# Performance work log

Measured on AMD Instinct MI355X. Metric: run time of the kernel, lower is better.

The kernel has to match this reference:

```python
import jax, jax.numpy as jnp
import numpy as np

D_MODEL = 1024
EXPAND = 2
D_INNER = EXPAND * D_MODEL   # 2048
D_STATE = 16
D_CONV = 4
DT_RANK = 64                  # ceil(d_model / 16)
BATCH = 2
SEQLEN = 1024
DT_MIN, DT_MAX = 0.001, 0.1


def setup_inputs() -> dict:
    key = jax.random.key(0)
    ks = jax.random.split(key, 10)
    s = 0.02
    # dt bias init per Mamba: inv-softplus of dt sampled log-uniform in [dt_min, dt_max]
    u = jax.random.uniform(ks[0], (D_INNER,), jnp.float32)
    dt = jnp.exp(u * (np.log(DT_MAX) - np.log(DT_MIN)) + np.log(DT_MIN))
    dt = jnp.clip(dt, 1e-4, None)
    inv_dt = dt + jnp.log(-jnp.expm1(-dt))
    dt_std = DT_RANK ** -0.5
    A_log = jnp.log(jnp.tile(jnp.arange(1, D_STATE + 1, dtype=jnp.float32), (D_INNER, 1)))
    return {
        "hidden_states": jax.random.normal(ks[1], (BATCH, SEQLEN, D_MODEL), jnp.float32),
        "in_proj_w": jax.random.normal(ks[2], (2 * D_INNER, D_MODEL), jnp.float32) * s,
        "conv1d_w": jax.random.normal(ks[3], (D_INNER, D_CONV), jnp.float32) * s,
        "conv1d_b": jnp.zeros((D_INNER,), jnp.float32),
        "x_proj_w": jax.random.normal(ks[4], (DT_RANK + 2 * D_STATE, D_INNER), jnp.float32) * s,
        "dt_proj_w": jax.random.uniform(ks[5], (D_INNER, DT_RANK), jnp.float32, -dt_std, dt_std),
        "dt_proj_b": inv_dt,
        "A_log": A_log,
        "D_skip": jnp.ones((D_INNER,), jnp.float32),
        "out_proj_w": jax.random.normal(ks[6], (D_MODEL, D_INNER), jnp.float32) * s,
    }


def _mamba_forward(hidden_states, in_proj_w, conv1d_w, conv1d_b, x_proj_w,
                   dt_proj_w, dt_proj_b, A_log, D_skip, out_proj_w):
    B_, L, _ = hidden_states.shape
    # in_proj: (b, l, d_model) -> (b, l, 2*d_inner); split into x and gate z
    xz = jnp.einsum('bld,ed->ble', hidden_states, in_proj_w)
    x, z = xz[..., :D_INNER], xz[..., D_INNER:]
    # causal depthwise conv1d over time (pad left K-1, truncate to L) + SiLU
    xp = jnp.pad(x, ((0, 0), (D_CONV - 1, 0), (0, 0)))
    xc = conv1d_b
    acc = jnp.zeros_like(x)
    for k in range(D_CONV):  # tiny fixed kernel loop
        acc = acc + conv1d_w[:, k] * xp[:, k:k + L, :]
    xc = jax.nn.silu(acc + conv1d_b)
    # input-dependent dt / B / C
    x_dbl = jnp.einsum('bld,rd->blr', xc, x_proj_w)
    dt_lr = x_dbl[..., :DT_RANK]
    Bm = x_dbl[..., DT_RANK:DT_RANK + D_STATE]        # (b, l, n)
    Cm = x_dbl[..., DT_RANK + D_STATE:]               # (b, l, n)
    delta = jax.nn.softplus(jnp.einsum('blr,dr->bld', dt_lr, dt_proj_w) + dt_proj_b)
    A = -jnp.exp(A_log)                               # (d, n)

    def step(state, inputs):
        delta_t, B_t, C_t, u_t = inputs               # (b,d) (b,n) (b,n) (b,d)
        dA = jnp.exp(delta_t[..., None] * A)          # (b, d, n)
        state = state * dA + (delta_t * u_t)[..., None] * B_t[:, None, :]
        y_t = jnp.einsum('bdn,bn->bd', state, C_t)
        return state, y_t

    init = jnp.zeros((B_, D_INNER, D_STATE), delta.dtype)
    scan_in = (jnp.swapaxes(delta, 0, 1), jnp.swapaxes(Bm, 0, 1),
               jnp.swapaxes(Cm, 0, 1), jnp.swapaxes(xc, 0, 1))
    _, ys = jax.lax.scan(step, init, scan_in)         # ys: (l, b, d)
    y = jnp.swapaxes(ys, 0, 1)
    y = y + xc * D_skip                               # skip connection
    y = y * jax.nn.silu(z)                            # gate
    return jnp.einsum('bld,md->blm', y, out_proj_w)   # out_proj (no bias)


def reference(hidden_states, in_proj_w, conv1d_w, conv1d_b, x_proj_w,
              dt_proj_w, dt_proj_b, A_log, D_skip, out_proj_w):
    return _mamba_forward(hidden_states, in_proj_w, conv1d_w, conv1d_b, x_proj_w,
                          dt_proj_w, dt_proj_b, A_log, D_skip, out_proj_w)
```

## Files before the change

### kernel.cpp

```cpp
#include <hip/hip_runtime.h>
#include <hip/hip_bf16.h>
#include <math.h>
#include <stdint.h>

#define D_MODEL 1024
#define D_INNER 2048
#define D_STATE 16
#define D_CONV  4
#define DT_RANK 64
#define BATCH   2
#define SEQLEN  1024
#define M_TOK   (BATCH * SEQLEN)
#define XDBL_W  (DT_RANK + 2 * D_STATE)
#define CHUNKS  64
#define CLEN    (SEQLEN / CHUNKS)
#define KSPLIT  32
#define OSPLIT  4

typedef unsigned short us16;
typedef __bf16 bf16x8 __attribute__((ext_vector_type(8)));
typedef float floatx4 __attribute__((ext_vector_type(4)));

__device__ __forceinline__ float silu_f(float v) {
    return v / (1.0f + __expf(-v));
}
__device__ __forceinline__ float softplus_f(float v) {
    return v > 20.0f ? v : log1pf(__expf(v));
}
__device__ __forceinline__ us16 f2bf(float f) {
    unsigned u = __float_as_uint(f);
    u += 0x7FFF + ((u >> 16) & 1);
    return (us16)(u >> 16);
}
__device__ __forceinline__ float bf2f(us16 h) {
    return __uint_as_float(((unsigned)h) << 16);
}

__device__ __forceinline__ void gload_lds16(const us16* g, us16* l) {
    auto* l3 = reinterpret_cast<__attribute__((address_space(3))) us16*>(
        reinterpret_cast<uintptr_t>(l));
    auto* g1 = reinterpret_cast<const __attribute__((address_space(1))) us16*>(
        reinterpret_cast<uintptr_t>(g));
    __builtin_amdgcn_global_load_lds(g1, l3, 16, 0, 0);
}

__global__ __launch_bounds__(256)
void split_all(const float* __restrict__ hs, const float* __restrict__ iw,
               const float* __restrict__ ow,
               us16* __restrict__ hsh, us16* __restrict__ hsl,
               us16* __restrict__ iwh, us16* __restrict__ iwl,
               us16* __restrict__ owh, us16* __restrict__ owl)
{
    const int b = blockIdx.x;
    const float* src;
    us16 *hi, *lo;
    int rel;
    if (b < 2048)      { src = hs; hi = hsh; lo = hsl; rel = b; }
    else if (b < 6144) { src = iw; hi = iwh; lo = iwl; rel = b - 2048; }
    else               { src = ow; hi = owh; lo = owl; rel = b - 6144; }
    const int i = (rel * 256 + threadIdx.x) * 4;
    const float4 v = *(const float4*)(src + i);
    us16 h0 = f2bf(v.x), h1 = f2bf(v.y), h2 = f2bf(v.z), h3 = f2bf(v.w);
    ushort4 hv = {h0, h1, h2, h3};
    ushort4 lv = {f2bf(v.x - bf2f(h0)), f2bf(v.y - bf2f(h1)),
                  f2bf(v.z - bf2f(h2)), f2bf(v.w - bf2f(h3))};
    *(ushort4*)(hi + i) = hv;
    *(ushort4*)(lo + i) = lv;
}

template<int BN, int MODE>
__global__ __launch_bounds__(256)
void gemm_mfma3(const us16* __restrict__ Ah, const us16* __restrict__ Al,
                const us16* __restrict__ Wh, const us16* __restrict__ Wl,
                int lda, int kLen, float* __restrict__ C0,
                float* __restrict__ C1, int ldc)
{
    constexpr int BM = 128;
    constexpr int NT = BN / 32;
    __shared__ us16 sAh[BM * 32];
    __shared__ us16 sAl[BM * 32];
    __shared__ us16 sWh[BN * 32];
    __shared__ us16 sWl[BN * 32];

    const int tid  = threadIdx.x;
    const int wave = tid >> 6;
    const int lane = tid & 63;
    const int wm   = wave & 1;
    const int wn   = wave >> 1;
    const int m0   = blockIdx.y * BM;
    const int n0   = blockIdx.x * BN;
    const int kBeg = blockIdx.z * kLen;
    const int quad = lane >> 4;
    const int l15  = lane & 15;
    const int sr   = lane >> 2;
    const int spos = lane & 3;

    floatx4 acc[4][NT] = {};

    for (int k0 = 0; k0 < kLen; k0 += 32) {
        __syncthreads();
        {
            int s = wave;
            int row = s * 16 + sr;
            int c = spos ^ ((row >> 1) & 3);
            size_t go = (size_t)(m0 + row) * lda + kBeg + k0 + c * 8;
            gload_lds16(Ah + go, sAh + s * 512);
            gload_lds16(Al + go, sAl + s * 512);
            s = wave + 4;
            row = s * 16 + sr;
            c = spos ^ ((row >> 1) & 3);
            go = (size_t)(m0 + row) * lda + kBeg + k0 + c * 8;
            gload_lds16(Ah + go, sAh + s * 512);
            gload_lds16(Al + go, sAl + s * 512);
        }
        {
            int s = wave;
            int row = s * 16 + sr;
            int c = spos ^ ((row >> 1) & 3);
            size_t go = (size_t)(n0 + row) * lda + kBeg + k0 + c * 8;
            gload_lds16(Wh + go, sWh + s * 512);
            gload_lds16(Wl + go, sWl + s * 512);
            if (BN == 128) {
                s = wave + 4;
                row = s * 16 + sr;
                c = spos ^ ((row >> 1) & 3);
                go = (size_t)(n0 + row) * lda + kBeg + k0 + c * 8;
                gload_lds16(Wh + go, sWh + s * 512);
                gload_lds16(Wl + go, sWl + s * 512);
            }
        }
        __syncthreads();

        bf16x8 ah[4], al[4], bh[NT], bl[NT];
#pragma unroll
        for (int i = 0; i < 4; i++) {
            const int r = wm * 64 + i * 16 + l15;
            const int off = r * 32 + ((quad ^ ((r >> 1) & 3)) * 8);
            ah[i] = *(const bf16x8*)(sAh + off);
            al[i] = *(const bf16x8*)(sAl + off);
        }
#pragma unroll
        for (int j = 0; j < NT; j++) {
            const int r = wn * (BN / 2) + j * 16 + l15;
            const int off = r * 32 + ((quad ^ ((r >> 1) & 3)) * 8);
            bh[j] = *(const bf16x8*)(sWh + off);
            bl[j] = *(const bf16x8*)(sWl + off);
        }
#pragma unroll
        for (int i = 0; i < 4; i++)
#pragma unroll
            for (int j = 0; j < NT; j++) {
                acc[i][j] = __builtin_amdgcn_mfma_f32_16x16x32_bf16(
                    ah[i], bh[j], acc[i][j], 0, 0, 0);
                acc[i][j] = __builtin_amdgcn_mfma_f32_16x16x32_bf16(
                    al[i], bh[j], acc[i][j], 0, 0, 0);
                acc[i][j] = __builtin_amdgcn_mfma_f32_16x16x32_bf16(
                    ah[i], bl[j], acc[i][j], 0, 0, 0);
            }
    }

#pragma unroll
    for (int i = 0; i < 4; i++) {
        const int rowb = m0 + wm * 64 + i * 16 + quad * 4;
#pragma unroll
        for (int j = 0; j < NT; j++) {
            const int col = n0 + wn * (BN / 2) + j * 16 + l15;
#pragma unroll
            for (int r = 0; r < 4; r++) {
                const float v = acc[i][j][r];
                const size_t rr = (size_t)(rowb + r);
                if (MODE == 1) {
                    if (n0 < D_INNER) C0[rr * D_INNER + col] = v;
                    else              C1[rr * D_INNER + (col - D_INNER)] = v;
                } else {
                    C0[((size_t)blockIdx.z * M_TOK + rr) * ldc + col] = v;
                }
            }
        }
    }
}

__global__ __launch_bounds__(256)
void add4_kernel(const float* __restrict__ part, float* __restrict__ out)
{
    const int i = (blockIdx.x * 256 + threadIdx.x) * 4;
    const size_t stride = (size_t)M_TOK * D_MODEL;
    float4 a = *(const float4*)(part + i);
#pragma unroll
    for (int k = 1; k < OSPLIT; k++) {
        const float4 b = *(const float4*)(part + k * stride + i);
        a.x += b.x; a.y += b.y; a.z += b.z; a.w += b.w;
    }
    *(float4*)(out + i) = a;
}

__global__ __launch_bounds__(256)
void gemm_dt(const float* __restrict__ A, int lda,
             const float* __restrict__ W, int ldw,
             float* __restrict__ C0, int ldc,
             const float* __restrict__ bias, int K)
{
    __shared__ float As[16][68];
    __shared__ float Ws[16][68];

    const int tid  = threadIdx.x;
    const int tx   = tid & 15;
    const int ty   = tid >> 4;
    const int n0   = blockIdx.x * 64;
    const int m0   = blockIdx.y * 64;
    const int lrow = tid >> 2;
    const int lkq  = tid & 3;

    float acc[4][4] = {};

    for (int k0 = 0; k0 < K; k0 += 16) {
        const float4 av = *(const float4*)(A + (size_t)(m0 + lrow) * lda + k0 + lkq * 4);
        const float4 wv = *(const float4*)(W + (size_t)(n0 + lrow) * ldw + k0 + lkq * 4);

        __syncthreads();
        As[lkq * 4 + 0][lrow] = av.x;
        As[lkq * 4 + 1][lrow] = av.y;
        As[lkq * 4 + 2][lrow] = av.z;
        As[lkq * 4 + 3][lrow] = av.w;
        Ws[lkq * 4 + 0][lrow] = wv.x;
        Ws[lkq * 4 + 1][lrow] = wv.y;
        Ws[lkq * 4 + 2][lrow] = wv.z;
        Ws[lkq * 4 + 3][lrow] = wv.w;
        __syncthreads();

#pragma unroll
        for (int k = 0; k < 16; k++) {
            const float4 a = *(const float4*)&As[k][ty * 4];
            const float4 w = *(const float4*)&Ws[k][tx * 4];
            const float avv[4] = {a.x, a.y, a.z, a.w};
            const float wvv[4] = {w.x, w.y, w.z, w.w};
#pragma unroll
            for (int i = 0; i < 4; i++)
#pragma unroll
                for (int j = 0; j < 4; j++)
                    acc[i][j] += avv[i] * wvv[j];
        }
    }

    const int mbase = m0 + ty * 4;
    const int nbase = n0 + tx * 4;
#pragma unroll
    for (int i = 0; i < 4; i++)
#pragma unroll
        for (int j = 0; j < 4; j++) {
            const int n = nbase + j;
            C0[(size_t)(mbase + i) * ldc + n] = softplus_f(acc[i][j] + bias[n]);
        }
}

__global__ __launch_bounds__(256)
void gemm_xproj(const float* __restrict__ xg, const float* __restrict__ conv_w,
                const float* __restrict__ conv_b,
                const float* __restrict__ W, float* __restrict__ part)
{
    __shared__ float As[16][68];
    __shared__ float Ws[16][100];

    const int tid  = threadIdx.x;
    const int tx   = tid & 15;
    const int ty   = tid >> 4;
    const int m0   = blockIdx.x * 64;
    const int kz   = blockIdx.y;
    const int lrow = tid >> 2;
    const int lkq  = tid & 3;

    const float4* cw = (const float4*)conv_w;
    const float4* cb = (const float4*)conv_b;

    float acc[4][6] = {};
    const int kbeg = kz * (D_INNER / KSPLIT);
    const int kend = kbeg + (D_INNER / KSPLIT);

    const int m = m0 + lrow;
    const int t = m & (SEQLEN - 1);

    for (int k0 = kbeg; k0 < kend; k0 += 16) {
        const int dcol = k0 + lkq * 4;
        const float4 w0 = cw[dcol], w1 = cw[dcol + 1], w2 = cw[dcol + 2], w3 = cw[dcol + 3];
        float4 a = cb[dcol >> 2];
        const float* xr = xg + (size_t)m * D_INNER + dcol;
        {
            float4 xk;
            if (t >= 3) { xk = *(const float4*)(xr - 3 * D_INNER);
                a.x += w0.x * xk.x; a.y += w1.x * xk.y; a.z += w2.x * xk.z; a.w += w3.x * xk.w; }
            if (t >= 2) { xk = *(const float4*)(xr - 2 * D_INNER);
                a.x += w0.y * xk.x; a.y += w1.y * xk.y; a.z += w2.y * xk.z; a.w += w3.y * xk.w; }
            if (t >= 1) { xk = *(const float4*)(xr - 1 * D_INNER);
                a.x += w0.z * xk.x; a.y += w1.z * xk.y; a.z += w2.z * xk.z; a.w += w3.z * xk.w; }
            xk = *(const float4*)(xr);
            a.x += w0.w * xk.x; a.y += w1.w * xk.y; a.z += w2.w * xk.z; a.w += w3.w * xk.w;
        }
        const float4 av = make_float4(silu_f(a.x), silu_f(a.y), silu_f(a.z), silu_f(a.w));

        const float4 wv = *(const float4*)(W + (size_t)lrow * D_INNER + k0 + lkq * 4);
        float4 wv2 = make_float4(0.f, 0.f, 0.f, 0.f);
        if (tid < 128)
            wv2 = *(const float4*)(W + (size_t)(64 + lrow) * D_INNER + k0 + lkq * 4);

        __syncthreads();
        As[lkq * 4 + 0][lrow] = av.x;
        As[lkq * 4 + 1][lrow] = av.y;
        As[lkq * 4 + 2][lrow] = av.z;
        As[lkq * 4 + 3][lrow] = av.w;
        Ws[lkq * 4 + 0][lrow] = wv.x;
        Ws[lkq * 4 + 1][lrow] = wv.y;
        Ws[lkq * 4 + 2][lrow] = wv.z;
        Ws[lkq * 4 + 3][lrow] = wv.w;
        if (tid < 128) {
            Ws[lkq * 4 + 0][64 + lrow] = wv2.x;
            Ws[lkq * 4 + 1][64 + lrow] = wv2.y;
            Ws[lkq * 4 + 2][64 + lrow] = wv2.z;
            Ws[lkq * 4 + 3][64 + lrow] = wv2.w;
        }
        __syncthreads();

#pragma unroll
        for (int k = 0; k < 16; k++) {
            const float4 a4 = *(const float4*)&As[k][ty * 4];
            const float avv[4] = {a4.x, a4.y, a4.z, a4.w};
            float wvv[6];
#pragma unroll
            for (int j = 0; j < 6; j++) wvv[j] = Ws[k][tx * 6 + j];
#pragma unroll
            for (int i = 0; i < 4; i++)
#pragma unroll
                for (int j = 0; j < 6; j++)
                    acc[i][j] += avv[i] * wvv[j];
        }
    }

    const int mbase = m0 + ty * 4;
    const int nbase = tx * 6;
#pragma unroll
    for (int i = 0; i < 4; i++)
#pragma unroll
        for (int j = 0; j < 6; j++)
            part[((size_t)kz * M_TOK + mbase + i) * XDBL_W + nbase + j] = acc[i][j];
}

__global__ __launch_bounds__(256)
void xproj_reduce(const float* __restrict__ part, float* __restrict__ xdbl)
{
    const int i = blockIdx.x * 256 + threadIdx.x;
    float s = 0.f;
#pragma unroll 8
    for (int k = 0; k < KSPLIT; k++)
        s += part[(size_t)k * M_TOK * XDBL_W + i];
    xdbl[i] = s;
}

__global__ __launch_bounds__(256)
void scan_part(const float* __restrict__ delta, const float* __restrict__ xdbl,
               const float* __restrict__ xg, const float* __restrict__ conv_w,
               const float* __restrict__ conv_b, const float* __restrict__ A_log,
               float* __restrict__ P, float* __restrict__ S)
{
    const int g = blockIdx.x * 256 + threadIdx.x;
    const int d = g & (D_INNER - 1);
    const int c = (g >> 11) & (CHUNKS - 1);
    const int b = g >> 17;

    float An[D_STATE];
#pragma unroll
    for (int n = 0; n < D_STATE; n++)
        An[n] = -__expf(A_log[d * D_STATE + n]);

    const float4 wd = ((const float4*)conv_w)[d];
    const float cb = conv_b[d];

    float p[D_STATE], s[D_STATE];
#pragma unroll
    for (int n = 0; n < D_STATE; n++) { p[n] = 1.f; s[n] = 0.f; }

    const size_t row0 = (size_t)b * SEQLEN + c * CLEN;
    const float* xp = xg + row0 * D_INNER + d;
    float xm3 = 0.f, xm2 = 0.f, xm1 = 0.f;
    if (c > 0) {
        xm3 = xp[-3 * D_INNER];
        xm2 = xp[-2 * D_INNER];
        xm1 = xp[-1 * D_INNER];
    }

#pragma unroll 4
    for (int t = 0; t < CLEN; t++) {
        const size_t row = row0 + t;
        const float xm0 = xp[(size_t)t * D_INNER];
        const float u   = silu_f(cb + wd.x * xm3 + wd.y * xm2 + wd.z * xm1 + wd.w * xm0);
        xm3 = xm2; xm2 = xm1; xm1 = xm0;
        const float dlt  = delta[row * D_INNER + d];
        const float dltu = dlt * u;
        const float4* Bp = (const float4*)(xdbl + row * XDBL_W + DT_RANK);
        const float4 B0 = Bp[0], B1 = Bp[1], B2 = Bp[2], B3 = Bp[3];
        const float Bv[D_STATE] = {B0.x, B0.y, B0.z, B0.w, B1.x, B1.y, B1.z, B1.w,
                                   B2.x, B2.y, B2.z, B2.w, B3.x, B3.y, B3.z, B3.w};
#pragma unroll
        for (int n = 0; n < D_STATE; n++) {
            const float a = __expf(dlt * An[n]);
            s[n] = s[n] * a + dltu * Bv[n];
            p[n] *= a;
        }
    }

    const size_t base = ((size_t)(b * CHUNKS + c) * D_STATE) * D_INNER + d;
#pragma unroll
    for (int n = 0; n < D_STATE; n++) {
        P[base + (size_t)n * D_INNER] = p[n];
        S[base + (size_t)n * D_INNER] = s[n];
    }
}

__global__ __launch_bounds__(256)
void scan_prefix(float* PH, const float* __restrict__ S)
{
    const int g = blockIdx.x * 256 + threadIdx.x;
    const int d = g & (D_INNER - 1);
    const int n = (g >> 11) & (D_STATE - 1);
    const int b = g >> 15;

    float h = 0.f;
    for (int c = 0; c < CHUNKS; c++) {
        const size_t idx = ((size_t)(b * CHUNKS + c) * D_STATE + n) * D_INNER + d;
        const float p = PH[idx];
        const float s = S[idx];
        PH[idx] = h;
        h = s + p * h;
    }
}

__global__ __launch_bounds__(256)
void scan_apply(const float* __restrict__ delta, const float* __restrict__ xdbl,
                const float* __restrict__ xg, const float* __restrict__ conv_w,
                const float* __restrict__ conv_b, const float* __restrict__ A_log,
                const float* __restrict__ D_skip,
                const float* __restrict__ H,
                const float* __restrict__ z,
                us16* __restrict__ yh, us16* __restrict__ yl)
{
    const int g = blockIdx.x * 256 + threadIdx.x;
    const int d = g & (D_INNER - 1);
    const int c = (g >> 11) & (CHUNKS - 1);
    const int b = g >> 17;

    float An[D_STATE];
#pragma unroll
    for (int n = 0; n < D_STATE; n++)
        An[n] = -__expf(A_log[d * D_STATE + n]);

    const float4 wd = ((const float4*)conv_w)[d];
    const float cb = conv_b[d];

    float st[D_STATE];
    const size_t hbase = ((size_t)(b * CHUNKS + c) * D_STATE) * D_INNER + d;
#pragma unroll
    for (int n = 0; n < D_STATE; n++)
        st[n] = H[hbase + (size_t)n * D_INNER];

    const float Dv = D_skip[d];
    const size_t row0 = (size_t)b * SEQLEN + c * CLEN;
    const float* xp = xg + row0 * D_INNER + d;
    float xm3 = 0.f, xm2 = 0.f, xm1 = 0.f;
    if (c > 0) {
        xm3 = xp[-3 * D_INNER];
        xm2 = xp[-2 * D_INNER];
        xm1 = xp[-1 * D_INNER];
    }

#pragma unroll 4
    for (int t = 0; t < CLEN; t++) {
        const size_t row = row0 + t;
        const float xm0 = xp[(size_t)t * D_INNER];
        const float u   = silu_f(cb + wd.x * xm3 + wd.y * xm2 + wd.z * xm1 + wd.w * xm0);
        xm3 = xm2; xm2 = xm1; xm1 = xm0;
        const float dlt  = delta[row * D_INNER + d];
        const float dltu = dlt * u;
        const float4* Bp = (const float4*)(xdbl + row * XDBL_W + DT_RANK);
        const float4 B0 = Bp[0], B1 = Bp[1], B2 = Bp[2], B3 = Bp[3];
        const float4* Cp = (const float4*)(xdbl + row * XDBL_W + DT_RANK + D_STATE);
        const float4 C0 = Cp[0], C1 = Cp[1], C2 = Cp[2], C3 = Cp[3];
        const float Bv[D_STATE] = {B0.x, B0.y, B0.z, B0.w, B1.x, B1.y, B1.z, B1.w,
                                   B2.x, B2.y, B2.z, B2.w, B3.x, B3.y, B3.z, B3.w};
        const float Cv[D_STATE] = {C0.x, C0.y, C0.z, C0.w, C1.x, C1.y, C1.z, C1.w,
                                   C2.x, C2.y, C2.z, C2.w, C3.x, C3.y, C3.z, C3.w};
        float y = 0.f;
#pragma unroll
        for (int n = 0; n < D_STATE; n++) {
            const float a = __expf(dlt * An[n]);
            st[n] = st[n] * a + dltu * Bv[n];
            y += st[n] * Cv[n];
        }
        const float yv = (y + u * Dv) * silu_f(z[row * D_INNER + d]);
        const us16 h = f2bf(yv);
        yh[row * D_INNER + d] = h;
        yl[row * D_INNER + d] = f2bf(yv - bf2f(h));
    }
}

extern "C" void kernel_launch(void* const* d_in, const int* in_sizes, int n_in,
                              void* d_out, int out_size, void* d_ws, size_t ws_size,
                              hipStream_t stream)
{
    const float* hs         = (const float*)d_in[0];
    const float* in_proj_w  = (const float*)d_in[1];
    const float* conv_w     = (const float*)d_in[2];
    const float* conv_b     = (const float*)d_in[3];
    const float* x_proj_w   = (const float*)d_in[4];
    const float* dt_proj_w  = (const float*)d_in[5];
    const float* dt_proj_b  = (const float*)d_in[6];
    const float* A_log      = (const float*)d_in[7];
    const float* D_skip     = (const float*)d_in[8];
    const float* out_proj_w = (const float*)d_in[9];
    float* out = (float*)d_out;

    char* base = (char*)d_ws;
    const size_t MB = 1u << 20;
    float* xbuf  = (float*)(base);
    float* zbuf  = (float*)(base + 16 * MB);
    float* opart = (float*)(base);
    float* dbuf  = (float*)(base + 32 * MB);
    float* xdbl  = (float*)(base + 48 * MB);
    us16*  iwh   = (us16*)(base + 49 * MB);
    us16*  iwl   = (us16*)(base + 57 * MB);
    float* part  = (float*)(base + 49 * MB);
    float* Pbuf  = (float*)(base + 49 * MB);
    us16*  hsh   = (us16*)(base + 65 * MB);
    us16*  hsl   = (us16*)(base + 69 * MB);
    float* Sbuf  = (float*)(base + 65 * MB);
    us16*  ybh   = (us16*)(base + 65 * MB);
    us16*  ybl   = (us16*)(base + 73 * MB);
    us16*  owh   = (us16*)(base + 81 * MB);
    us16*  owl   = (us16*)(base + 85 * MB);

    const dim3 blk(256);

    split_all<<<8192, blk, 0, stream>>>(hs, in_proj_w, out_proj_w,
                                        hsh, hsl, iwh, iwl, owh, owl);

    gemm_mfma3<64, 1><<<dim3((2 * D_INNER) / 64, M_TOK / 128), blk, 0, stream>>>(
        hsh, hsl, iwh, iwl, D_MODEL, D_MODEL, xbuf, zbuf, D_INNER);

    gemm_xproj<<<dim3(M_TOK / 64, KSPLIT), blk, 0, stream>>>(
        xbuf, conv_w, conv_b, x_proj_w, part);
    xproj_reduce<<<(M_TOK * XDBL_W) / 256, blk, 0, stream>>>(part, xdbl);

    gemm_dt<<<dim3(D_INNER / 64, M_TOK / 64), blk, 0, stream>>>(
        xdbl, XDBL_W, dt_proj_w, DT_RANK, dbuf, D_INNER, dt_proj_b, DT_RANK);

    scan_part<<<(BATCH * CHUNKS * D_INNER) / 256, blk, 0, stream>>>(
        dbuf, xdbl, xbuf, conv_w, conv_b, A_log, Pbuf, Sbuf);
    scan_prefix<<<(BATCH * D_STATE * D_INNER) / 256, blk, 0, stream>>>(
        Pbuf, Sbuf);
    scan_apply<<<(BATCH * CHUNKS * D_INNER) / 256, blk, 0, stream>>>(
        dbuf, xdbl, xbuf, conv_w, conv_b, A_log, D_skip, Pbuf, zbuf, ybh, ybl);

    gemm_mfma3<128, 2><<<dim3(D_MODEL / 128, M_TOK / 128, OSPLIT), blk, 0, stream>>>(
        ybh, ybl, owh, owl, D_INNER, D_INNER / OSPLIT, opart, nullptr, D_MODEL);
    add4_kernel<<<(M_TOK * D_MODEL) / 1024, blk, 0, stream>>>(opart, out);
}
```

Baseline: 323.6 us.

## Replace split-K partial buffers and reduce kernels with atomic accumulation

The out_proj and x_proj split-K GEMMs now accumulate straight into the output and xdbl with float atomicAdd, after a new kernel zeroes both buffers. This removes the add4 and xproj_reduce kernels and their partial-buffer traffic. The in_proj GEMM also moves from a 64-wide to a 128-wide N tile, giving fewer blocks with more reuse. In exchange, the 32-way atomic contention on the small xdbl buffer may be costly, and the summation order is no longer deterministic.

```diff
diff --git a/kernel.cpp b/kernel.cpp
--- a/kernel.cpp
+++ b/kernel.cpp
@@ -42,6 +42,19 @@
     auto* g1 = reinterpret_cast<const __attribute__((address_space(1))) us16*>(
         reinterpret_cast<uintptr_t>(g));
     __builtin_amdgcn_global_load_lds(g1, l3, 16, 0, 0);
+}
+
+__global__ __launch_bounds__(256)
+void zero_kernel(float* __restrict__ out, float* __restrict__ xdbl)
+{
+    const int b = blockIdx.x;
+    if (b < 2048) {
+        const int i = (b * 256 + threadIdx.x) * 4;
+        *(float4*)(out + i) = make_float4(0.f, 0.f, 0.f, 0.f);
+    } else {
+        const int i = ((b - 2048) * 256 + threadIdx.x) * 4;
+        *(float4*)(xdbl + i) = make_float4(0.f, 0.f, 0.f, 0.f);
+    }
 }
 
 __global__ __launch_bounds__(256)
@@ -120,14 +133,12 @@
             size_t go = (size_t)(n0 + row) * lda + kBeg + k0 + c * 8;
             gload_lds16(Wh + go, sWh + s * 512);
             gload_lds16(Wl + go, sWl + s * 512);
-            if (BN == 128) {
-                s = wave + 4;
-                row = s * 16 + sr;
-                c = spos ^ ((row >> 1) & 3);
-                go = (size_t)(n0 + row) * lda + kBeg + k0 + c * 8;
-                gload_lds16(Wh + go, sWh + s * 512);
-                gload_lds16(Wl + go, sWl + s * 512);
-            }
+            s = wave + 4;
+            row = s * 16 + sr;
+            c = spos ^ ((row >> 1) & 3);
+            go = (size_t)(n0 + row) * lda + kBeg + k0 + c * 8;
+            gload_lds16(Wh + go, sWh + s * 512);
+            gload_lds16(Wl + go, sWl + s * 512);
         }
         __syncthreads();
 
@@ -173,25 +184,11 @@
                     if (n0 < D_INNER) C0[rr * D_INNER + col] = v;
                     else              C1[rr * D_INNER + (col - D_INNER)] = v;
                 } else {
-                    C0[((size_t)blockIdx.z * M_TOK + rr) * ldc + col] = v;
+                    atomicAdd(&C0[rr * ldc + col], v);
                 }
             }
         }
     }
-}
-
-__global__ __launch_bounds__(256)
-void add4_kernel(const float* __restrict__ part, float* __restrict__ out)
-{
-    const int i = (blockIdx.x * 256 + threadIdx.x) * 4;
-    const size_t stride = (size_t)M_TOK * D_MODEL;
-    float4 a = *(const float4*)(part + i);
-#pragma unroll
-    for (int k = 1; k < OSPLIT; k++) {
-        const float4 b = *(const float4*)(part + k * stride + i);
-        a.x += b.x; a.y += b.y; a.z += b.z; a.w += b.w;
-    }
-    *(float4*)(out + i) = a;
 }
 
 __global__ __launch_bounds__(256)
@@ -256,7 +253,7 @@
 __global__ __launch_bounds__(256)
 void gemm_xproj(const float* __restrict__ xg, const float* __restrict__ conv_w,
                 const float* __restrict__ conv_b,
-                const float* __restrict__ W, float* __restrict__ part)
+                const float* __restrict__ W, float* __restrict__ xdbl)
 {
     __shared__ float As[16][68];
     __shared__ float Ws[16][100];
@@ -340,18 +337,7 @@
     for (int i = 0; i < 4; i++)
 #pragma unroll
         for (int j = 0; j < 6; j++)
-            part[((size_t)kz * M_TOK + mbase + i) * XDBL_W + nbase + j] = acc[i][j];
-}
-
-__global__ __launch_bounds__(256)
-void xproj_reduce(const float* __restrict__ part, float* __restrict__ xdbl)
-{
-    const int i = blockIdx.x * 256 + threadIdx.x;
-    float s = 0.f;
-#pragma unroll 8
-    for (int k = 0; k < KSPLIT; k++)
-        s += part[(size_t)k * M_TOK * XDBL_W + i];
-    xdbl[i] = s;
+            atomicAdd(&xdbl[(size_t)(mbase + i) * XDBL_W + nbase + j], acc[i][j]);
 }
 
 __global__ __launch_bounds__(256)
@@ -520,12 +506,10 @@
     const size_t MB = 1u << 20;
     float* xbuf  = (float*)(base);
     float* zbuf  = (float*)(base + 16 * MB);
-    float* opart = (float*)(base);
     float* dbuf  = (float*)(base + 32 * MB);
     float* xdbl  = (float*)(base + 48 * MB);
     us16*  iwh   = (us16*)(base + 49 * MB);
     us16*  iwl   = (us16*)(base + 57 * MB);
-    float* part  = (float*)(base + 49 * MB);
     float* Pbuf  = (float*)(base + 49 * MB);
     us16*  hsh   = (us16*)(base + 65 * MB);
     us16*  hsl   = (us16*)(base + 69 * MB);
@@ -537,15 +521,16 @@
 
     const dim3 blk(256);
 
+    zero_kernel<<<2048 + (M_TOK * XDBL_W) / 1024, blk, 0, stream>>>(out, xdbl);
+
     split_all<<<8192, blk, 0, stream>>>(hs, in_proj_w, out_proj_w,
                                         hsh, hsl, iwh, iwl, owh, owl);
 
-    gemm_mfma3<64, 1><<<dim3((2 * D_INNER) / 64, M_TOK / 128), blk, 0, stream>>>(
+    gemm_mfma3<128, 1><<<dim3((2 * D_INNER) / 128, M_TOK / 128), blk, 0, stream>>>(
         hsh, hsl, iwh, iwl, D_MODEL, D_MODEL, xbuf, zbuf, D_INNER);
 
     gemm_xproj<<<dim3(M_TOK / 64, KSPLIT), blk, 0, stream>>>(
-        xbuf, conv_w, conv_b, x_proj_w, part);
-    xproj_reduce<<<(M_TOK * XDBL_W) / 256, blk, 0, stream>>>(part, xdbl);
+        xbuf, conv_w, conv_b, x_proj_w, xdbl);
 
     gemm_dt<<<dim3(D_INNER / 64, M_TOK / 64), blk, 0, stream>>>(
         xdbl, XDBL_W, dt_proj_w, DT_RANK, dbuf, D_INNER, dt_proj_b, DT_RANK);
@@ -558,6 +543,5 @@
         dbuf, xdbl, xbuf, conv_w, conv_b, A_log, D_skip, Pbuf, zbuf, ybh, ybl);
 
     gemm_mfma3<128, 2><<<dim3(D_MODEL / 128, M_TOK / 128, OSPLIT), blk, 0, stream>>>(
-        ybh, ybl, owh, owl, D_INNER, D_INNER / OSPLIT, opart, nullptr, D_MODEL);
-    add4_kernel<<<(M_TOK * D_MODEL) / 1024, blk, 0, stream>>>(opart, out);
-}
+        ybh, ybl, owh, owl, D_INNER, D_INNER / OSPLIT, out, nullptr, D_MODEL);
+}
```

Result: slower. 446.3 us (+37.9%).
